# Kernel tuning notes

Measured on AMD Instinct MI355X. Metric: run time of the kernel, lower is better.

The kernel has to match this reference:

```python
import jax, jax.numpy as jnp
import numpy as np

N_NODES = 100000
N_EDGES = 1600000
IN_FEATS = 128
OUT_FEATS = 128


def setup_inputs() -> dict:
    key = jax.random.key(0)
    k1, k2, k3, k4, k5 = jax.random.split(key, 5)
    feature = jax.random.normal(k1, (N_NODES, IN_FEATS), dtype=jnp.float32)
    src = jax.random.randint(k2, (N_EDGES,), 0, N_NODES, dtype=jnp.int64)
    dst = jax.random.randint(k3, (N_EDGES,), 0, N_NODES, dtype=jnp.int64)
    # nn.Linear default init: U(-1/sqrt(in), 1/sqrt(in)); randn scaled is fine for a numeric baseline
    bound = 1.0 / np.sqrt(IN_FEATS)
    W = jax.random.uniform(k4, (OUT_FEATS, IN_FEATS), dtype=jnp.float32, minval=-bound, maxval=bound)
    b = jax.random.uniform(k5, (OUT_FEATS,), dtype=jnp.float32, minval=-bound, maxval=bound)
    return {"feature": feature, "src": src, "dst": dst, "W": W, "b": b}


def reference(feature, src, dst, W, b):
    # message passing: copy source feature along each edge, sum into destination node
    agg = jax.ops.segment_sum(feature[src], dst, num_segments=N_NODES)  # [N, in_feats]
    # node apply: ReLU(Linear(h))
    return jax.nn.relu(agg @ W.T + b)  # [N, out_feats]
```

## Files before the change

### kernel.cpp

```cpp
#include <hip/hip_runtime.h>

#define N_NODES 100000
#define N_EDGES 1600000
#define F 128

#define NB    1563
#define NBP2  2048
#define CAP   1280
#define CHUNK 8192

#define BIN_BLOCKS  196
#define FEAT_BLOCKS 3125
#define WCONV_BLOCKS 16
#define FRONT_GRID  (BIN_BLOCKS + FEAT_BLOCKS + WCONV_BLOCKS)

typedef __bf16  bf16x8 __attribute__((ext_vector_type(8)));
typedef float   f32x4  __attribute__((ext_vector_type(4)));

__device__ inline unsigned short f32_to_bf16(float f) {
    unsigned u = __builtin_bit_cast(unsigned, f);
    u += 0x7FFFu + ((u >> 16) & 1u);
    return (unsigned short)(u >> 16);
}
__device__ inline unsigned pack_bf16x2(float lo, float hi) {
    return (unsigned)f32_to_bf16(lo) | ((unsigned)f32_to_bf16(hi) << 16);
}
__device__ inline void addrow(float* acc, const uint4 v) {
    acc[0] += __builtin_bit_cast(float, v.x << 16);
    acc[1] += __builtin_bit_cast(float, v.x & 0xFFFF0000u);
    acc[2] += __builtin_bit_cast(float, v.y << 16);
    acc[3] += __builtin_bit_cast(float, v.y & 0xFFFF0000u);
    acc[4] += __builtin_bit_cast(float, v.z << 16);
    acc[5] += __builtin_bit_cast(float, v.z & 0xFFFF0000u);
    acc[6] += __builtin_bit_cast(float, v.w << 16);
    acc[7] += __builtin_bit_cast(float, v.w & 0xFFFF0000u);
}

__global__ __launch_bounds__(1024) void gcn_front(
    const float* __restrict__ feat, const float* __restrict__ W,
    const int* __restrict__ src, const int* __restrict__ dst,
    int* __restrict__ gcur, unsigned* __restrict__ bins,
    unsigned short* __restrict__ Wbf, float* __restrict__ out)
{
    __shared__ unsigned cnt[NBP2];
    __shared__ unsigned off[NBP2];
    __shared__ int      gbase[NBP2];
    __shared__ unsigned staged[CHUNK];
    __shared__ unsigned short sbk[CHUNK];
    __shared__ unsigned scan[1024];

    const int tid = threadIdx.x;
    const int bx  = blockIdx.x;

    if (bx >= BIN_BLOCKS) {
        const int rb = bx - BIN_BLOCKS;
        if (rb < FEAT_BLOCKS) {
            const int t = rb * 1024 + tid;
            const float4 v = *(const float4*)(feat + (size_t)t * 4);
            uint2 p;
            p.x = pack_bf16x2(v.x, v.y);
            p.y = pack_bf16x2(v.z, v.w);
            const int n = t >> 5, q = t & 31;
            *(uint2*)((char*)out + (size_t)n * 512 + q * 8) = p;
        } else {
            const int i = (rb - FEAT_BLOCKS) * 1024 + tid;
            Wbf[i] = f32_to_bf16(W[i]);
        }
        return;
    }

    const int e0 = bx * CHUNK;

    #pragma unroll
    for (int i = 0; i < 2; ++i) cnt[tid + i * 1024] = 0;
    __syncthreads();

    int sv[8], dv[8];
    #pragma unroll
    for (int i = 0; i < 8; ++i) {
        const int e = e0 + tid + i * 1024;
        if (e < N_EDGES) {
            sv[i] = src[e];
            dv[i] = dst[e];
            atomicAdd(&cnt[dv[i] >> 6], 1u);
        } else dv[i] = -1;
    }
    __syncthreads();

    const unsigned s = cnt[2 * tid] + cnt[2 * tid + 1];
    scan[tid] = s;
    __syncthreads();
    for (int o = 1; o < 1024; o <<= 1) {
        const unsigned t = (tid >= o) ? scan[tid - o] : 0;
        __syncthreads();
        scan[tid] += t;
        __syncthreads();
    }
    const unsigned run = scan[tid] - s;
    off[2 * tid]     = run;
    off[2 * tid + 1] = run + cnt[2 * tid];
    __syncthreads();

    #pragma unroll
    for (int i = 0; i < 8; ++i) {
        if (dv[i] >= 0) {
            const int bk = dv[i] >> 6;
            const unsigned w = (unsigned)sv[i] | ((unsigned)(dv[i] & 63) << 17);
            const unsigned p = atomicAdd(&off[bk], 1u);
            staged[p] = w;
            sbk[p] = (unsigned short)bk;
        }
    }
    __syncthreads();

    #pragma unroll
    for (int i = 0; i < 2; ++i) {
        const int bk = 2 * tid + i;
        if (bk < NB && cnt[bk] > 0)
            gbase[bk] = atomicAdd(&gcur[bk], (int)cnt[bk]);
    }
    __syncthreads();

    const int c_tot = (int)scan[1023];
    for (int p = tid; p < c_tot; p += 1024) {
        const int bk = sbk[p];
        const int gp = gbase[bk] + (p - (int)(off[bk] - cnt[bk]));
        if (gp < CAP) bins[(size_t)bk * CAP + gp] = staged[p];
    }
}

__global__ __launch_bounds__(512) void gcn_accum2(
    const int* __restrict__ gcur,
    const unsigned* __restrict__ bins,
    float* __restrict__ out)
{
    __shared__ unsigned tmp[CAP];
    __shared__ unsigned list[CAP];
    __shared__ int cnt64[64], scn[64], pos64[64], cur64[64];

    const int tid = threadIdx.x;
    const int bkt = blockIdx.x;

    int c = gcur[bkt]; if (c > CAP) c = CAP;
    const unsigned* bb = bins + (size_t)bkt * CAP;

    for (int i = tid; i < c; i += 512) tmp[i] = bb[i];
    if (tid < 64) cnt64[tid] = 0;
    __syncthreads();

    for (int i = tid; i < c; i += 512) atomicAdd(&cnt64[(tmp[i] >> 17) & 63], 1);
    __syncthreads();

    if (tid < 64) scn[tid] = cnt64[tid];
    __syncthreads();
    #pragma unroll
    for (int o = 1; o < 64; o <<= 1) {
        int t = 0;
        if (tid < 64 && tid >= o) t = scn[tid - o];
        __syncthreads();
        if (tid < 64) scn[tid] += t;
        __syncthreads();
    }
    if (tid < 64) {
        const int st = scn[tid] - cnt64[tid];
        pos64[tid] = st;
        cur64[tid] = st;
    }
    __syncthreads();

    for (int i = tid; i < c; i += 512) {
        const unsigned w = tmp[i];
        const int p = atomicAdd(&cur64[(w >> 17) & 63], 1);
        list[p] = w;
    }
    __syncthreads();

    const int grp = tid >> 4;
    const int sl  = tid & 15;
    const int n0  = bkt * 64;

    #pragma unroll
    for (int ni = 0; ni < 2; ++ni) {
        const int l  = grp * 2 + ni;
        const int st = pos64[l];
        const int en = st + cnt64[l];

        float a0[8] = {0,0,0,0,0,0,0,0};
        float a1[8] = {0,0,0,0,0,0,0,0};
        int k = st;
        for (; k + 3 < en; k += 4) {
            const unsigned w0 = list[k],     w1 = list[k + 1];
            const unsigned w2 = list[k + 2], w3 = list[k + 3];
            const uint4 v0 = *(const uint4*)((const char*)out + (size_t)(w0 & 0x1FFFF) * 512 + sl * 16);
            const uint4 v1 = *(const uint4*)((const char*)out + (size_t)(w1 & 0x1FFFF) * 512 + sl * 16);
            const uint4 v2 = *(const uint4*)((const char*)out + (size_t)(w2 & 0x1FFFF) * 512 + sl * 16);
            const uint4 v3 = *(const uint4*)((const char*)out + (size_t)(w3 & 0x1FFFF) * 512 + sl * 16);
            addrow(a0, v0); addrow(a1, v1); addrow(a0, v2); addrow(a1, v3);
        }
        for (; k < en; ++k) {
            const unsigned w0 = list[k];
            const uint4 v0 = *(const uint4*)((const char*)out + (size_t)(w0 & 0x1FFFF) * 512 + sl * 16);
            addrow(a0, v0);
        }
        #pragma unroll
        for (int q = 0; q < 8; ++q) a0[q] += a1[q];

        const int n = n0 + l;
        if (n < N_NODES) {
            uint4 o;
            o.x = pack_bf16x2(a0[0], a0[1]);
            o.y = pack_bf16x2(a0[2], a0[3]);
            o.z = pack_bf16x2(a0[4], a0[5]);
            o.w = pack_bf16x2(a0[6], a0[7]);
            *(uint4*)((char*)out + (size_t)n * 512 + 256 + sl * 16) = o;
        }
    }
}

#define MT   128
#define LDP  136

__global__ __launch_bounds__(256) void gcn_gemm_mfma(
    float* __restrict__ out,
    const unsigned short* __restrict__ Wbf,
    const float* __restrict__ b)
{
    __shared__ unsigned short Alds[MT * LDP];
    __shared__ unsigned short Wlds[F * LDP];

    const int tid  = threadIdx.x;
    const int row0 = blockIdx.x * MT;

    #pragma unroll
    for (int i = 0; i < 8; ++i) {
        const int c = tid + i * 256;
        const int r = c >> 4, cc = c & 15;
        *(uint4*)&Wlds[r * LDP + cc * 8] = *(const uint4*)&Wbf[c * 8];
    }
    #pragma unroll
    for (int i = 0; i < 8; ++i) {
        const int c = tid + i * 256;
        const int r = c >> 4, cc = c & 15;
        int gr = row0 + r; if (gr > N_NODES - 1) gr = N_NODES - 1;
        const uint4 v = *(const uint4*)((const char*)out + (size_t)gr * 512 + 256 + cc * 16);
        *(uint4*)&Alds[r * LDP + cc * 8] = v;
    }
    __syncthreads();

    const int lane = tid & 63;
    const int wv   = tid >> 6;
    const int lr   = lane & 15;
    const int lq   = lane >> 4;

    f32x4 acc[2][8] = {};
    #pragma unroll
    for (int kk = 0; kk < 4; ++kk) {
        bf16x8 a[2], w[8];
        #pragma unroll
        for (int i = 0; i < 2; ++i)
            a[i] = __builtin_bit_cast(bf16x8,
                *(const uint4*)&Alds[(wv * 32 + i * 16 + lr) * LDP + kk * 32 + lq * 8]);
        #pragma unroll
        for (int n = 0; n < 8; ++n)
            w[n] = __builtin_bit_cast(bf16x8,
                *(const uint4*)&Wlds[(n * 16 + lr) * LDP + kk * 32 + lq * 8]);
        #pragma unroll
        for (int i = 0; i < 2; ++i)
            #pragma unroll
            for (int n = 0; n < 8; ++n)
                acc[i][n] = __builtin_amdgcn_mfma_f32_16x16x32_bf16(a[i], w[n], acc[i][n], 0, 0, 0);
    }

    float bias[8];
    #pragma unroll
    for (int n = 0; n < 8; ++n) bias[n] = b[n * 16 + lr];

    #pragma unroll
    for (int i = 0; i < 2; ++i) {
        const int rbase = wv * 32 + i * 16 + lq * 4;
        #pragma unroll
        for (int rg = 0; rg < 4; ++rg) {
            const int gr = row0 + rbase + rg;
            if (gr < N_NODES) {
                float* orow = out + (size_t)gr * F;
                #pragma unroll
                for (int n = 0; n < 8; ++n) {
                    const float v = acc[i][n][rg] + bias[n];
                    orow[n * 16 + lr] = v > 0.0f ? v : 0.0f;
                }
            }
        }
    }
}

__global__ __launch_bounds__(256) void gcn_scatter(
    const float* __restrict__ feat,
    const int* __restrict__ src, const int* __restrict__ dst,
    float* __restrict__ agg)
{
    const int sub  = threadIdx.x >> 5;
    const int lane = threadIdx.x & 31;
    const long long e = (long long)blockIdx.x * 8 + sub;
    if (e >= N_EDGES) return;
    const int s = src[e], d = dst[e];
    const float4 v = *(const float4*)(feat + (size_t)s * F + lane * 4);
    float* ar = agg + (size_t)d * F + lane * 4;
    unsafeAtomicAdd(ar + 0, v.x);
    unsafeAtomicAdd(ar + 1, v.y);
    unsafeAtomicAdd(ar + 2, v.z);
    unsafeAtomicAdd(ar + 3, v.w);
}

#define GR  64
#define LDW 132
__global__ __launch_bounds__(256) void gcn_gemm_relu(
    float* __restrict__ agg_out,
    const float* __restrict__ W, const float* __restrict__ b)
{
    __shared__ float Wl[F][LDW];
    __shared__ float At[GR][LDW];
    const int tid = threadIdx.x;
    const long long row0 = (long long)blockIdx.x * GR;
    #pragma unroll
    for (int i = 0; i < 64; ++i) {
        const int e = tid + i * 256;
        Wl[e >> 7][e & 127] = W[e];
    }
    #pragma unroll
    for (int i = 0; i < 32; ++i) {
        const int e = tid + i * 256;
        const int r = e >> 7, k2 = e & 127;
        const long long gr = row0 + r;
        At[r][k2] = (gr < N_NODES) ? agg_out[gr * F + k2] : 0.0f;
    }
    __syncthreads();
    const int tx = tid & 15, ty = tid >> 4, r0 = ty * 4;
    float acc[4][8];
    #pragma unroll
    for (int r = 0; r < 4; ++r)
        #pragma unroll
        for (int m = 0; m < 8; ++m) acc[r][m] = 0.0f;
    for (int k0 = 0; k0 < F; k0 += 4) {
        float4 a[4], w[8];
        #pragma unroll
        for (int r = 0; r < 4; ++r) a[r] = *(const float4*)&At[r0 + r][k0];
        #pragma unroll
        for (int m = 0; m < 8; ++m) w[m] = *(const float4*)&Wl[tx + 16 * m][k0];
        #pragma unroll
        for (int r = 0; r < 4; ++r)
            #pragma unroll
            for (int m = 0; m < 8; ++m)
                acc[r][m] += a[r].x * w[m].x + a[r].y * w[m].y
                           + a[r].z * w[m].z + a[r].w * w[m].w;
    }
    float bias[8];
    #pragma unroll
    for (int m = 0; m < 8; ++m) bias[m] = b[tx + 16 * m];
    __syncthreads();
    #pragma unroll
    for (int r = 0; r < 4; ++r) {
        const long long gr = row0 + r0 + r;
        if (gr < N_NODES) {
            float* orow = agg_out + gr * F;
            #pragma unroll
            for (int m = 0; m < 8; ++m) {
                const float v = acc[r][m] + bias[m];
                orow[tx + 16 * m] = v > 0.0f ? v : 0.0f;
            }
        }
    }
}

extern "C" void kernel_launch(void* const* d_in, const int* in_sizes, int n_in,
                              void* d_out, int out_size, void* d_ws, size_t ws_size,
                              hipStream_t stream) {
    const float* feat = (const float*)d_in[0];
    const int*   src  = (const int*)d_in[1];
    const int*   dst  = (const int*)d_in[2];
    const float* W    = (const float*)d_in[3];
    const float* b    = (const float*)d_in[4];
    float* out = (float*)d_out;

    const size_t ws_need = 1600u * 4 + (size_t)NB * CAP * 4 + (size_t)F * F * 2;

    if (ws_size >= ws_need) {
        int* gcur = (int*)d_ws;
        unsigned* bins = (unsigned*)(gcur + 1600);
        unsigned short* Wbf = (unsigned short*)(bins + (size_t)NB * CAP);

        hipMemsetAsync(gcur, 0, NB * sizeof(int), stream);
        gcn_front   <<<FRONT_GRID, 1024, 0, stream>>>(feat, W, src, dst, gcur, bins, Wbf, out);
        gcn_accum2  <<<NB, 512, 0, stream>>>(gcur, bins, out);
        gcn_gemm_mfma<<<(N_NODES + MT - 1) / MT, 256, 0, stream>>>(out, Wbf, b);
    } else {
        hipMemsetAsync(out, 0, (size_t)N_NODES * F * sizeof(float), stream);
        gcn_scatter<<<N_EDGES / 8, 256, 0, stream>>>(feat, src, dst, out);
        gcn_gemm_relu<<<(N_NODES + GR - 1) / GR, 256, 0, stream>>>(out, W, b);
    }
}
```

Before: 192.7 us.

## Apply linear transform before aggregation and fuse bias/ReLU into accumulation

Uses linearity to compute H = feature·Wᵀ in bf16 with MFMA inside the front kernel, alongside the edge-binning blocks. The aggregation kernel then gathers rows of H, adds bias, applies ReLU and writes fp32 output directly, which removes the separate GEMM kernel and the intermediate write and read of aggregated features. It needs a larger workspace for H (N×128 bf16) and falls back to the old path when the workspace is too small. Rounding H to bf16 before summation changes where precision is lost.

```diff
diff --git a/kernel.cpp b/kernel.cpp
--- a/kernel.cpp
+++ b/kernel.cpp
@@ -9,10 +9,12 @@
 #define CAP   1280
 #define CHUNK 8192
 
-#define BIN_BLOCKS  196
-#define FEAT_BLOCKS 3125
-#define WCONV_BLOCKS 16
-#define FRONT_GRID  (BIN_BLOCKS + FEAT_BLOCKS + WCONV_BLOCKS)
+#define BIN_BLOCKS   196
+#define HGEMM_BLOCKS 782
+#define FRONT_GRID_LIN (BIN_BLOCKS + HGEMM_BLOCKS)
+
+#define LDP  136
+#define SMEM_BYTES 77824
 
 typedef __bf16  bf16x8 __attribute__((ext_vector_type(8)));
 typedef float   f32x4  __attribute__((ext_vector_type(4)));
@@ -35,6 +37,256 @@
     acc[6] += __builtin_bit_cast(float, v.w << 16);
     acc[7] += __builtin_bit_cast(float, v.w & 0xFFFF0000u);
 }
+
+__global__ __launch_bounds__(1024) void gcn_front_lin(
+    const float* __restrict__ feat, const float* __restrict__ W,
+    const int* __restrict__ src, const int* __restrict__ dst,
+    int* __restrict__ gcur, unsigned* __restrict__ bins,
+    unsigned short* __restrict__ H)
+{
+    __shared__ __align__(16) unsigned char smem[SMEM_BYTES];
+
+    const int tid = threadIdx.x;
+    const int bx  = blockIdx.x;
+
+    if (bx >= BIN_BLOCKS) {
+        unsigned short* Alds = (unsigned short*)smem;
+        unsigned short* Wlds = Alds + 128 * LDP;
+        const int row0 = (bx - BIN_BLOCKS) * 128;
+
+        #pragma unroll
+        for (int i = 0; i < 4; ++i) {
+            const int c = tid + i * 1024;
+            const int r = c >> 5, cc = c & 31;
+            const float4 v = *(const float4*)(W + (size_t)c * 4);
+            uint2 p; p.x = pack_bf16x2(v.x, v.y); p.y = pack_bf16x2(v.z, v.w);
+            *(uint2*)&Wlds[r * LDP + cc * 4] = p;
+        }
+        #pragma unroll
+        for (int i = 0; i < 4; ++i) {
+            const int c = tid + i * 1024;
+            const int r = c >> 5, cc = c & 31;
+            int gr = row0 + r; if (gr > N_NODES - 1) gr = N_NODES - 1;
+            const float4 v = *(const float4*)(feat + (size_t)gr * F + cc * 4);
+            uint2 p; p.x = pack_bf16x2(v.x, v.y); p.y = pack_bf16x2(v.z, v.w);
+            *(uint2*)&Alds[r * LDP + cc * 4] = p;
+        }
+        __syncthreads();
+
+        const int lane = tid & 63, wv = tid >> 6;
+        const int lr = lane & 15, lq = lane >> 4;
+        const int wr = wv & 7;
+        const int wc = wv >> 3;
+
+        f32x4 acc[4] = {};
+        #pragma unroll
+        for (int kk = 0; kk < 4; ++kk) {
+            const bf16x8 a = __builtin_bit_cast(bf16x8,
+                *(const uint4*)&Alds[(wr * 16 + lr) * LDP + kk * 32 + lq * 8]);
+            #pragma unroll
+            for (int n2 = 0; n2 < 4; ++n2) {
+                const bf16x8 w = __builtin_bit_cast(bf16x8,
+                    *(const uint4*)&Wlds[((wc * 4 + n2) * 16 + lr) * LDP + kk * 32 + lq * 8]);
+                acc[n2] = __builtin_amdgcn_mfma_f32_16x16x32_bf16(a, w, acc[n2], 0, 0, 0);
+            }
+        }
+        #pragma unroll
+        for (int rg = 0; rg < 4; ++rg) {
+            const int gr = row0 + wr * 16 + lq * 4 + rg;
+            if (gr < N_NODES) {
+                unsigned short* hrow = H + (size_t)gr * F;
+                #pragma unroll
+                for (int n2 = 0; n2 < 4; ++n2)
+                    hrow[(wc * 4 + n2) * 16 + lr] = f32_to_bf16(acc[n2][rg]);
+            }
+        }
+        return;
+    }
+
+    unsigned*       cnt    = (unsigned*)smem;
+    unsigned*       off    = cnt + NBP2;
+    int*            gbase  = (int*)(off + NBP2);
+    unsigned*       staged = (unsigned*)(gbase + NBP2);
+    unsigned short* sbk    = (unsigned short*)(staged + CHUNK);
+    unsigned*       scan   = (unsigned*)(sbk + CHUNK);
+
+    const int e0 = bx * CHUNK;
+
+    #pragma unroll
+    for (int i = 0; i < 2; ++i) cnt[tid + i * 1024] = 0;
+    __syncthreads();
+
+    int sv[8], dv[8];
+    #pragma unroll
+    for (int i = 0; i < 8; ++i) {
+        const int e = e0 + tid + i * 1024;
+        if (e < N_EDGES) {
+            sv[i] = src[e];
+            dv[i] = dst[e];
+            atomicAdd(&cnt[dv[i] >> 6], 1u);
+        } else dv[i] = -1;
+    }
+    __syncthreads();
+
+    const unsigned s = cnt[2 * tid] + cnt[2 * tid + 1];
+    scan[tid] = s;
+    __syncthreads();
+    for (int o = 1; o < 1024; o <<= 1) {
+        const unsigned t = (tid >= o) ? scan[tid - o] : 0;
+        __syncthreads();
+        scan[tid] += t;
+        __syncthreads();
+    }
+    const unsigned run = scan[tid] - s;
+    off[2 * tid]     = run;
+    off[2 * tid + 1] = run + cnt[2 * tid];
+    __syncthreads();
+
+    #pragma unroll
+    for (int i = 0; i < 8; ++i) {
+        if (dv[i] >= 0) {
+            const int bk = dv[i] >> 6;
+            const unsigned w = (unsigned)sv[i] | ((unsigned)(dv[i] & 63) << 17);
+            const unsigned p = atomicAdd(&off[bk], 1u);
+            staged[p] = w;
+            sbk[p] = (unsigned short)bk;
+        }
+    }
+    __syncthreads();
+
+    #pragma unroll
+    for (int i = 0; i < 2; ++i) {
+        const int bk = 2 * tid + i;
+        if (bk < NB && cnt[bk] > 0)
+            gbase[bk] = atomicAdd(&gcur[bk], (int)cnt[bk]);
+    }
+    __syncthreads();
+
+    const int c_tot = (int)scan[1023];
+    for (int p = tid; p < c_tot; p += 1024) {
+        const int bk = sbk[p];
+        const int gp = gbase[bk] + (p - (int)(off[bk] - cnt[bk]));
+        if (gp < CAP) bins[(size_t)bk * CAP + gp] = staged[p];
+    }
+}
+
+__global__ __launch_bounds__(512) void gcn_accum_lin(
+    const int* __restrict__ gcur,
+    const unsigned* __restrict__ bins,
+    const unsigned short* __restrict__ H,
+    const float* __restrict__ b,
+    float* __restrict__ out)
+{
+    __shared__ unsigned tmp[CAP];
+    __shared__ unsigned list[CAP];
+    __shared__ int cnt64[64], scn[64], pos64[64], cur64[64];
+
+    const int tid = threadIdx.x;
+    const int bkt = blockIdx.x;
+
+    int c = gcur[bkt]; if (c > CAP) c = CAP;
+    const unsigned* bb = bins + (size_t)bkt * CAP;
+
+    for (int i = tid; i < c; i += 512) tmp[i] = bb[i];
+    if (tid < 64) cnt64[tid] = 0;
+    __syncthreads();
+
+    for (int i = tid; i < c; i += 512) atomicAdd(&cnt64[(tmp[i] >> 17) & 63], 1);
+    __syncthreads();
+
+    if (tid < 64) scn[tid] = cnt64[tid];
+    __syncthreads();
+    #pragma unroll
+    for (int o = 1; o < 64; o <<= 1) {
+        int t = 0;
+        if (tid < 64 && tid >= o) t = scn[tid - o];
+        __syncthreads();
+        if (tid < 64) scn[tid] += t;
+        __syncthreads();
+    }
+    if (tid < 64) {
+        const int st = scn[tid] - cnt64[tid];
+        pos64[tid] = st;
+        cur64[tid] = st;
+    }
+    __syncthreads();
+
+    for (int i = tid; i < c; i += 512) {
+        const unsigned w = tmp[i];
+        const int p = atomicAdd(&cur64[(w >> 17) & 63], 1);
+        list[p] = w;
+    }
+    __syncthreads();
+
+    const int grp = tid >> 4;
+    const int sl  = tid & 15;
+    const int n0  = bkt * 64;
+
+    #pragma unroll
+    for (int ni = 0; ni < 2; ++ni) {
+        const int l  = grp * 2 + ni;
+        const int st = pos64[l];
+        const int en = st + cnt64[l];
+
+        float a0[8] = {0,0,0,0,0,0,0,0};
+        float a1[8] = {0,0,0,0,0,0,0,0};
+        int k = st;
+        for (; k + 7 < en; k += 8) {
+            const unsigned w0 = list[k],     w1 = list[k + 1];
+            const unsigned w2 = list[k + 2], w3 = list[k + 3];
+            const unsigned w4 = list[k + 4], w5 = list[k + 5];
+            const unsigned w6 = list[k + 6], w7 = list[k + 7];
+            const uint4 v0 = *(const uint4*)(H + (size_t)(w0 & 0x1FFFF) * F + sl * 8);
+            const uint4 v1 = *(const uint4*)(H + (size_t)(w1 & 0x1FFFF) * F + sl * 8);
+            const uint4 v2 = *(const uint4*)(H + (size_t)(w2 & 0x1FFFF) * F + sl * 8);
+            const uint4 v3 = *(const uint4*)(H + (size_t)(w3 & 0x1FFFF) * F + sl * 8);
+            const uint4 v4 = *(const uint4*)(H + (size_t)(w4 & 0x1FFFF) * F + sl * 8);
+            const uint4 v5 = *(const uint4*)(H + (size_t)(w5 & 0x1FFFF) * F + sl * 8);
+            const uint4 v6 = *(const uint4*)(H + (size_t)(w6 & 0x1FFFF) * F + sl * 8);
+            const uint4 v7 = *(const uint4*)(H + (size_t)(w7 & 0x1FFFF) * F + sl * 8);
+            addrow(a0, v0); addrow(a1, v1); addrow(a0, v2); addrow(a1, v3);
+            addrow(a0, v4); addrow(a1, v5); addrow(a0, v6); addrow(a1, v7);
+        }
+        for (; k + 3 < en; k += 4) {
+            const unsigned w0 = list[k],     w1 = list[k + 1];
+            const unsigned w2 = list[k + 2], w3 = list[k + 3];
+            const uint4 v0 = *(const uint4*)(H + (size_t)(w0 & 0x1FFFF) * F + sl * 8);
+            const uint4 v1 = *(const uint4*)(H + (size_t)(w1 & 0x1FFFF) * F + sl * 8);
+            const uint4 v2 = *(const uint4*)(H + (size_t)(w2 & 0x1FFFF) * F + sl * 8);
+            const uint4 v3 = *(const uint4*)(H + (size_t)(w3 & 0x1FFFF) * F + sl * 8);
+            addrow(a0, v0); addrow(a1, v1); addrow(a0, v2); addrow(a1, v3);
+        }
+        for (; k < en; ++k) {
+            const unsigned w0 = list[k];
+            const uint4 v0 = *(const uint4*)(H + (size_t)(w0 & 0x1FFFF) * F + sl * 8);
+            addrow(a0, v0);
+        }
+        #pragma unroll
+        for (int q = 0; q < 8; ++q) a0[q] += a1[q];
+
+        const int n = n0 + l;
+        if (n < N_NODES) {
+            const float4 b0 = *(const float4*)(b + sl * 8);
+            const float4 b1 = *(const float4*)(b + sl * 8 + 4);
+            float4 o0, o1;
+            o0.x = fmaxf(a0[0] + b0.x, 0.0f);
+            o0.y = fmaxf(a0[1] + b0.y, 0.0f);
+            o0.z = fmaxf(a0[2] + b0.z, 0.0f);
+            o0.w = fmaxf(a0[3] + b0.w, 0.0f);
+            o1.x = fmaxf(a0[4] + b1.x, 0.0f);
+            o1.y = fmaxf(a0[5] + b1.y, 0.0f);
+            o1.z = fmaxf(a0[6] + b1.z, 0.0f);
+            o1.w = fmaxf(a0[7] + b1.w, 0.0f);
+            float* orow = out + (size_t)n * F + sl * 8;
+            *(float4*)orow = o0;
+            *(float4*)(orow + 4) = o1;
+        }
+    }
+}
+
+#define FEAT_BLOCKS 3125
+#define WCONV_BLOCKS 16
+#define FRONT_GRID  (BIN_BLOCKS + FEAT_BLOCKS + WCONV_BLOCKS)
 
 __global__ __launch_bounds__(1024) void gcn_front(
     const float* __restrict__ feat, const float* __restrict__ W,
@@ -218,7 +470,6 @@
 }
 
 #define MT   128
-#define LDP  136
 
 __global__ __launch_bounds__(256) void gcn_gemm_mfma(
     float* __restrict__ out,
@@ -381,9 +632,18 @@
     const float* b    = (const float*)d_in[4];
     float* out = (float*)d_out;
 
-    const size_t ws_need = 1600u * 4 + (size_t)NB * CAP * 4 + (size_t)F * F * 2;
-
-    if (ws_size >= ws_need) {
+    const size_t ws_lin = 1600u * 4 + (size_t)NB * CAP * 4 + (size_t)N_NODES * F * 2;
+    const size_t ws_old = 1600u * 4 + (size_t)NB * CAP * 4 + (size_t)F * F * 2;
+
+    if (ws_size >= ws_lin) {
+        int* gcur = (int*)d_ws;
+        unsigned* bins = (unsigned*)(gcur + 1600);
+        unsigned short* H = (unsigned short*)(bins + (size_t)NB * CAP);
+
+        hipMemsetAsync(gcur, 0, NB * sizeof(int), stream);
+        gcn_front_lin<<<FRONT_GRID_LIN, 1024, 0, stream>>>(feat, W, src, dst, gcur, bins, H);
+        gcn_accum_lin<<<NB, 512, 0, stream>>>(gcur, bins, H, b, out);
+    } else if (ws_size >= ws_old) {
         int* gcur = (int*)d_ws;
         unsigned* bins = (unsigned*)(gcur + 1600);
         unsigned short* Wbf = (unsigned short*)(bins + (size_t)NB * CAP);
```

After: 191.4 us. About the same (-0.7%).
